# Kernel optimization log

Hardware: AMD Instinct MI355X
Metric: run time of the kernel (lower is better)

## Reference

```python
import jax, jax.numpy as jnp
import numpy as np

N_USERS = 100_000
N_ITEMS = 50_000
E = 2_000_000
B = 100_000
DU, DI, H, L = 256, 128, 64, 2
EPS = 1e-5  # BatchNorm eps


def setup_inputs() -> dict:
    key = jax.random.key(0)
    ks = jax.random.split(key, 32)
    f32 = jnp.float32
    inp = {
        "user_features": jax.random.normal(ks[0], (N_USERS, DU), f32),
        "item_features": jax.random.normal(ks[1], (N_ITEMS, DI), f32),
        "edge_index": jnp.stack([
            jax.random.randint(ks[2], (E,), 0, N_USERS),
            jax.random.randint(ks[3], (E,), 0, N_ITEMS),
        ]).astype(jnp.int32),
        "edge_label_index": jnp.stack([
            jax.random.randint(ks[4], (B,), 0, N_USERS),
            jax.random.randint(ks[5], (B,), 0, N_ITEMS),
        ]).astype(jnp.int32),
        # projections (stored as [in, out])
        "user_proj_W": jax.random.normal(ks[6], (DU, H), f32) * 0.05,
        "user_proj_b": jax.random.normal(ks[7], (H,), f32) * 0.05,
        "item_proj_W": jax.random.normal(ks[8], (DI, H), f32) * 0.05,
        "item_proj_b": jax.random.normal(ks[9], (H,), f32) * 0.05,
        # SAGEConv weights stacked over layers: lin_l (aggr neighbors, with bias), lin_r (self, no bias)
        "u_lin_l_W": jax.random.normal(ks[10], (L, H, H), f32) * 0.1,
        "u_lin_l_b": jax.random.normal(ks[11], (L, H), f32) * 0.05,
        "u_lin_r_W": jax.random.normal(ks[12], (L, H, H), f32) * 0.1,
        "i_lin_l_W": jax.random.normal(ks[13], (L, H, H), f32) * 0.1,
        "i_lin_l_b": jax.random.normal(ks[14], (L, H), f32) * 0.05,
        "i_lin_r_W": jax.random.normal(ks[15], (L, H, H), f32) * 0.1,
        # BatchNorm (eval mode: affine + running stats)
        "u_bn_gamma": 1.0 + jax.random.normal(ks[16], (L, H), f32) * 0.05,
        "u_bn_beta": jax.random.normal(ks[17], (L, H), f32) * 0.05,
        "u_bn_mean": jax.random.normal(ks[18], (L, H), f32) * 0.05,
        "u_bn_var": jax.random.uniform(ks[19], (L, H), f32, 0.5, 1.5),
        "i_bn_gamma": 1.0 + jax.random.normal(ks[20], (L, H), f32) * 0.05,
        "i_bn_beta": jax.random.normal(ks[21], (L, H), f32) * 0.05,
        "i_bn_mean": jax.random.normal(ks[22], (L, H), f32) * 0.05,
        "i_bn_var": jax.random.uniform(ks[23], (L, H), f32, 0.5, 1.5),
        # final MLP head
        "fc1_W": jax.random.normal(ks[24], (2 * H, H), f32) * 0.1,
        "fc1_b": jax.random.normal(ks[25], (H,), f32) * 0.05,
        "fc2_W": jax.random.normal(ks[26], (H, 4), f32) * 0.1,
        "fc2_b": jax.random.normal(ks[27], (4,), f32) * 0.05,
    }
    return inp


def _bn(x, g, b, m, v):
    return (x - m) * (g * jax.lax.rsqrt(v + EPS)) + b


def _forward(user_features, item_features, edge_index, edge_label_index,
             user_proj_W, user_proj_b, item_proj_W, item_proj_b,
             u_lin_l_W, u_lin_l_b, u_lin_r_W,
             i_lin_l_W, i_lin_l_b, i_lin_r_W,
             u_bn_gamma, u_bn_beta, u_bn_mean, u_bn_var,
             i_bn_gamma, i_bn_beta, i_bn_mean, i_bn_var,
             fc1_W, fc1_b, fc2_W, fc2_b):
    src, dst = edge_index[0], edge_index[1]  # user idx, item idx
    ux = user_features @ user_proj_W + user_proj_b  # [Nu, H]
    ix = item_features @ item_proj_W + item_proj_b  # [Ni, H]
    # in-degree of items (for mean aggregation), clamp for isolated nodes
    deg_i = jnp.clip(jax.ops.segment_sum(jnp.ones((E,), ux.dtype), dst, N_ITEMS), 1.0)[:, None]
    for l in range(L):
        # user conv: aggr='max' over item neighbors (edge_index flipped)
        agg_u = jax.ops.segment_max(ix[dst], src, num_segments=N_USERS)
        agg_u = jnp.where(jnp.isfinite(agg_u), agg_u, 0.0)  # empty segments -> 0 (PyG behavior)
        u_new = agg_u @ u_lin_l_W[l] + u_lin_l_b[l] + ux @ u_lin_r_W[l]
        u_new = jax.nn.relu(_bn(u_new, u_bn_gamma[l], u_bn_beta[l], u_bn_mean[l], u_bn_var[l]))
        # item conv: aggr='mean' over user neighbors
        agg_i = jax.ops.segment_sum(ux[src], dst, num_segments=N_ITEMS) / deg_i
        i_new = agg_i @ i_lin_l_W[l] + i_lin_l_b[l] + ix @ i_lin_r_W[l]
        i_new = jax.nn.relu(_bn(i_new, i_bn_gamma[l], i_bn_beta[l], i_bn_mean[l], i_bn_var[l]))
        ux, ix = u_new, i_new
    uh = ux[edge_label_index[0]]  # [B, H]
    ih = ix[edge_label_index[1]]  # [B, H]
    x = jnp.concatenate([uh, ih], axis=1)  # [B, 2H]
    return jax.nn.relu(x @ fc1_W + fc1_b) @ fc2_W + fc2_b  # [B, 4]


def reference(user_features, item_features, edge_index, edge_label_index,
              user_proj_W, user_proj_b, item_proj_W, item_proj_b,
              u_lin_l_W, u_lin_l_b, u_lin_r_W,
              i_lin_l_W, i_lin_l_b, i_lin_r_W,
              u_bn_gamma, u_bn_beta, u_bn_mean, u_bn_var,
              i_bn_gamma, i_bn_beta, i_bn_mean, i_bn_var,
              fc1_W, fc1_b, fc2_W, fc2_b):
    return _forward(user_features, item_features, edge_index, edge_label_index,
                    user_proj_W, user_proj_b, item_proj_W, item_proj_b,
                    u_lin_l_W, u_lin_l_b, u_lin_r_W,
                    i_lin_l_W, i_lin_l_b, i_lin_r_W,
                    u_bn_gamma, u_bn_beta, u_bn_mean, u_bn_var,
                    i_bn_gamma, i_bn_beta, i_bn_mean, i_bn_var,
                    fc1_W, fc1_b, fc2_W, fc2_b)
```

## Files before the change

### kernel.cpp

```cpp
#include <hip/hip_runtime.h>
#include <math.h>

#define N_USERS 100000
#define N_ITEMS 50000
#define NE      2000000
#define NB      100000
#define H       64
#define BN_EPS  1e-5f
#define P_PART  8
#define U_LOC   (N_USERS / P_PART)
#define I_LOC   (N_ITEMS / P_PART)
#define HSLOTS  (U_LOC + I_LOC)
#define S_SLICES 50
#define NBLK_CSR (P_PART * S_SLICES)
#define E_SLICE  (NE / S_SLICES)
#define Q_SLICE  (E_SLICE / 4)
#define SCAN_CHUNK 2048
#define T_CSR   512
#define GU_BLK  ((N_USERS + 127) / 128)
#define GI_BLK  ((N_ITEMS + 127) / 128)

typedef __attribute__((ext_vector_type(8))) short bf16x8;
typedef __attribute__((ext_vector_type(4))) float f32x4;
typedef __attribute__((ext_vector_type(4))) int   i32x4;

static __device__ __forceinline__ int rfl(int x) { return __builtin_amdgcn_readfirstlane(x); }

static __device__ __forceinline__ unsigned short f2bf(float f) {
  union { float f; unsigned u; } v; v.f = f;
  const unsigned r = v.u + 0x7fffu + ((v.u >> 16) & 1u);
  return (unsigned short)(r >> 16);
}
static __device__ __forceinline__ float bf2f(unsigned short h) {
  union { unsigned u; float f; } v; v.u = (unsigned)h << 16;
  return v.f;
}
static __device__ __forceinline__ float bfu_lo(unsigned x) {
  union { unsigned u; float f; } v; v.u = x << 16;
  return v.f;
}
static __device__ __forceinline__ float bfu_hi(unsigned x) {
  union { unsigned u; float f; } v; v.u = x & 0xffff0000u;
  return v.f;
}

__global__ __launch_bounds__(256) void pack_kernel(
    const float* __restrict__ upW, const float* __restrict__ ipW,
    const float* __restrict__ ulW, const float* __restrict__ urW,
    const float* __restrict__ ilW, const float* __restrict__ irW,
    const float* __restrict__ f1W, unsigned short* __restrict__ dst) {
  const int b = blockIdx.x;
  const int ct = threadIdx.x >> 6, lane = threadIdx.x & 63;
  const float* src;
  int krow0;
  if (b < 8)       { src = upW; krow0 = b * 32; }
  else if (b < 12) { src = ipW; krow0 = (b - 8) * 32; }
  else if (b < 28) {
    const int idx = b - 12, t = idx >> 2, ks = idx & 3;
    const int layer = t & 1;
    const float* Wl = (t < 2) ? ulW : ilW;
    const float* Wr = (t < 2) ? urW : irW;
    src = ((ks < 2) ? Wl : Wr) + layer * 4096;
    krow0 = ((ks < 2) ? ks : ks - 2) * 32;
  } else { src = f1W; krow0 = (b - 28) * 32; }
  unsigned short* out = dst + (size_t)b * 2048 + ((size_t)ct * 64 + lane) * 8;
  const int col = ct * 16 + (lane & 15);
  const int kr = krow0 + (lane >> 4) * 8;
#pragma unroll
  for (int j = 0; j < 8; j++) out[j] = f2bf(src[(kr + j) * 64 + col]);
}

template<int K>
static __device__ __forceinline__ void proj_body(
    const float* __restrict__ X, const unsigned short* __restrict__ Wf,
    const float* __restrict__ bias, unsigned short* __restrict__ Y,
    int nrows, int bp) {
  const int lane = threadIdx.x & 63;
  const int wave = rfl((int)(threadIdx.x >> 6));
  const int r0 = (bp * 8 + wave) * 16;
  if (r0 >= nrows) return;
  const int arow = r0 + (lane & 15);
  const int ar = arow < nrows ? arow : nrows - 1;
  const int k0 = (lane >> 4) * 8;
  f32x4 acc[4] = {};
#pragma unroll
  for (int ks = 0; ks < K / 32; ks++) {
    const float* xp = X + (size_t)ar * K + ks * 32 + k0;
    const float4 xa = *reinterpret_cast<const float4*>(xp);
    const float4 xb = *reinterpret_cast<const float4*>(xp + 4);
    bf16x8 af;
    af[0] = f2bf(xa.x); af[1] = f2bf(xa.y); af[2] = f2bf(xa.z); af[3] = f2bf(xa.w);
    af[4] = f2bf(xb.x); af[5] = f2bf(xb.y); af[6] = f2bf(xb.z); af[7] = f2bf(xb.w);
#pragma unroll
    for (int ct = 0; ct < 4; ct++) {
      const bf16x8 bfr = *reinterpret_cast<const bf16x8*>(
          Wf + ((size_t)(ks * 4 + ct) * 64 + lane) * 8);
      acc[ct] = __builtin_amdgcn_mfma_f32_16x16x32_bf16(af, bfr, acc[ct], 0, 0, 0);
    }
  }
  const int orow0 = r0 + (lane >> 4) * 4;
#pragma unroll
  for (int ct = 0; ct < 4; ct++) {
    const int col = ct * 16 + (lane & 15);
    const float bv = bias[col];
#pragma unroll
    for (int i = 0; i < 4; i++) {
      const int r = orow0 + i;
      if (r < nrows) Y[(size_t)r * 64 + col] = f2bf(acc[ct][i] + bv);
    }
  }
}

__global__ __launch_bounds__(T_CSR) void fused_hist_proj(
    const int* __restrict__ src, const int* __restrict__ dst,
    unsigned short* __restrict__ PH,
    const float* __restrict__ userF, const float* __restrict__ itemF,
    const unsigned short* __restrict__ wpack,
    const float* __restrict__ upb, const float* __restrict__ ipb,
    unsigned short* __restrict__ ux0, unsigned short* __restrict__ ix0) {
  __shared__ int h[HSLOTS];
  const int b = blockIdx.x;
  if (b < NBLK_CSR) {
    const int p = b & (P_PART - 1);
    const int s = b >> 3;
    for (int i = threadIdx.x; i < HSLOTS; i += T_CSR) h[i] = 0;
    __syncthreads();
    const int uLo = p * U_LOC, iLo = p * I_LOC;
    const int e0 = s * E_SLICE;
    const i32x4* s4 = reinterpret_cast<const i32x4*>(src + e0);
    const i32x4* d4 = reinterpret_cast<const i32x4*>(dst + e0);
    for (int i = threadIdx.x; i < Q_SLICE; i += T_CSR) {
      const i32x4 us = s4[i];
      const i32x4 ds = d4[i];
#pragma unroll
      for (int q = 0; q < 4; q++) {
        const int ul = us[q] - uLo;
        if ((unsigned)ul < (unsigned)U_LOC) atomicAdd(&h[ul], 1);
        const int il = ds[q] - iLo;
        if ((unsigned)il < (unsigned)I_LOC) atomicAdd(&h[U_LOC + il], 1);
      }
    }
    __syncthreads();
    unsigned short* out = PH + (size_t)b * HSLOTS;
    for (int i = threadIdx.x; i < HSLOTS; i += T_CSR)
      __builtin_nontemporal_store((unsigned short)h[i], &out[i]);
  } else if (b < NBLK_CSR + GU_BLK) {
    proj_body<256>(userF, wpack, upb, ux0, N_USERS, b - NBLK_CSR);
  } else {
    proj_body<128>(itemF, wpack + 8 * 2048, ipb, ix0, N_ITEMS,
                   b - NBLK_CSR - GU_BLK);
  }
}

__global__ __launch_bounds__(256) void conv_mfma(
    const unsigned short* __restrict__ AGG, const unsigned short* __restrict__ XS,
    const unsigned short* __restrict__ Wf, const float* __restrict__ bl,
    const float* __restrict__ gm, const float* __restrict__ bt,
    const float* __restrict__ mu, const float* __restrict__ vr,
    unsigned short* __restrict__ Y, int nrows) {
  const int lane = threadIdx.x & 63;
  const int wave = rfl((int)(threadIdx.x >> 6));
  const int r0 = (blockIdx.x * 4 + wave) * 16;
  if (r0 >= nrows) return;
  const int arow = r0 + (lane & 15);
  const int ar = arow < nrows ? arow : nrows - 1;
  const int k0 = (lane >> 4) * 8;
  f32x4 acc[4] = {};
#pragma unroll
  for (int ks = 0; ks < 4; ks++) {
    const unsigned short* ap =
        (ks < 2 ? AGG : XS) + (size_t)ar * 64 + (ks & 1) * 32 + k0;
    const bf16x8 af = *reinterpret_cast<const bf16x8*>(ap);
#pragma unroll
    for (int ct = 0; ct < 4; ct++) {
      const bf16x8 bfr = *reinterpret_cast<const bf16x8*>(
          Wf + ((size_t)(ks * 4 + ct) * 64 + lane) * 8);
      acc[ct] = __builtin_amdgcn_mfma_f32_16x16x32_bf16(af, bfr, acc[ct], 0, 0, 0);
    }
  }
  const int orow0 = r0 + (lane >> 4) * 4;
#pragma unroll
  for (int ct = 0; ct < 4; ct++) {
    const int col = ct * 16 + (lane & 15);
    const float s = gm[col] * rsqrtf(vr[col] + BN_EPS);
    const float C = (bl[col] - mu[col]) * s + bt[col];
#pragma unroll
    for (int i = 0; i < 4; i++) {
      const int r = orow0 + i;
      if (r < nrows)
        Y[(size_t)r * 64 + col] = f2bf(fmaxf(fmaf(acc[ct][i], s, C), 0.f));
    }
  }
}

__global__ __launch_bounds__(256) void combine_kernel(
    unsigned short* __restrict__ PH, int* __restrict__ cntU,
    int* __restrict__ cntI) {
  const int g = blockIdx.x * 256 + threadIdx.x;
  if (g >= P_PART * HSLOTS) return;
  const int x = g / HSLOTS;
  const int n = g - x * HSLOTS;
  unsigned short* p = PH + (size_t)x * HSLOTS + n;
  int run = 0;
#pragma unroll 2
  for (int s = 0; s < S_SLICES; s++) {
    unsigned short* q = p + (size_t)s * (P_PART * HSLOTS);
    const int v = (int)__builtin_nontemporal_load(q);
    __builtin_nontemporal_store((unsigned short)run, q);
    run += v;
  }
  if (n < U_LOC) cntU[x * U_LOC + n] = run;
  else           cntI[x * I_LOC + (n - U_LOC)] = run;
}

__global__ __launch_bounds__(256) void scan1_kernel(
    const int* __restrict__ cnt, int* __restrict__ row,
    int* __restrict__ bsum, int n) {
  __shared__ int wtot[4];
  const int tid = threadIdx.x;
  const int lane = tid & 63, wv = tid >> 6;
  const int i0 = blockIdx.x * SCAN_CHUNK + tid * 8;
  int sacc[8];
  int run = 0;
#pragma unroll
  for (int k = 0; k < 8; k++) {
    const int v = (i0 + k < n) ? cnt[i0 + k] : 0;
    run += v;
    sacc[k] = run;
  }
  int x = run;
#pragma unroll
  for (int off = 1; off < 64; off <<= 1) {
    const int y = __shfl_up(x, off);
    if (lane >= off) x += y;
  }
  if (lane == 63) wtot[wv] = x;
  __syncthreads();
  int woff = 0;
#pragma unroll
  for (int k = 0; k < 4; k++) woff += (k < wv) ? wtot[k] : 0;
  const int excl = (x - run) + woff;
#pragma unroll
  for (int k = 0; k < 8; k++)
    if (i0 + k < n) row[i0 + k + 1] = excl + sacc[k];
  if (tid == 255) bsum[blockIdx.x] = excl + run;
}

__global__ __launch_bounds__(256) void scan3_kernel(
    const int* __restrict__ bsum, int* __restrict__ row, int n) {
  __shared__ int off_s;
  const int b = blockIdx.x;
  const int tid = threadIdx.x;
  if (tid < 64) {
    int v = (tid < b) ? bsum[tid] : 0;
#pragma unroll
    for (int off = 32; off; off >>= 1) v += __shfl_xor(v, off);
    if (tid == 0) off_s = v;
  }
  __syncthreads();
  const int off = off_s;
  if (b == 0) {
    if (tid == 0) row[0] = 0;
    return;
  }
  const int i0 = b * SCAN_CHUNK + tid * 8;
#pragma unroll
  for (int k = 0; k < 8; k++)
    if (i0 + k < n) row[i0 + k + 1] += off;
}

__global__ __launch_bounds__(T_CSR) void scatter2_kernel(
    const int* __restrict__ src, const int* __restrict__ dst,
    const unsigned short* __restrict__ PH, const int* __restrict__ rowU,
    const int* __restrict__ rowI, int* __restrict__ adjU,
    int* __restrict__ adjI) {
  __shared__ int pos[HSLOTS];
  const int p = blockIdx.x & (P_PART - 1);
  const int s = blockIdx.x >> 3;
  const int uLo = p * U_LOC, iLo = p * I_LOC;
  const unsigned short* pre = PH + (size_t)blockIdx.x * HSLOTS;
  for (int i = threadIdx.x; i < U_LOC; i += T_CSR)
    pos[i] = rowU[uLo + i] + (int)__builtin_nontemporal_load(&pre[i]);
  for (int i = threadIdx.x; i < I_LOC; i += T_CSR)
    pos[U_LOC + i] = rowI[iLo + i] + (int)__builtin_nontemporal_load(&pre[U_LOC + i]);
  __syncthreads();
  const int e0 = s * E_SLICE;
  const i32x4* s4 = reinterpret_cast<const i32x4*>(src + e0);
  const i32x4* d4 = reinterpret_cast<const i32x4*>(dst + e0);
  for (int i = threadIdx.x; i < Q_SLICE; i += T_CSR) {
    const i32x4 us = s4[i];
    const i32x4 ds = d4[i];
#pragma unroll
    for (int q = 0; q < 4; q++) {
      const int u = us[q], it = ds[q];
      const int ul = u - uLo, il = it - iLo;
      if ((unsigned)ul < (unsigned)U_LOC) {
        const int pp = atomicAdd(&pos[ul], 1);
        adjU[pp] = it;
      }
      if ((unsigned)il < (unsigned)I_LOC) {
        const int pp = atomicAdd(&pos[U_LOC + il], 1);
        adjI[pp] = u;
      }
    }
  }
}

__global__ __launch_bounds__(256) void agg_max_kernel(
    const unsigned short* __restrict__ feat, const int* __restrict__ rowptr,
    const int* __restrict__ adj, unsigned short* __restrict__ out, int nseg) {
  const int lane = threadIdx.x & 63;
  const int wid  = rfl((int)(threadIdx.x >> 6));
  const int g    = lane >> 4;
  const int c4   = (lane & 15) * 4;
  for (int s = blockIdx.x * 4 + wid; s < nseg; s += gridDim.x * 4) {
    const int beg = rowptr[s], end = rowptr[s + 1];
    float m0 = -INFINITY, m1 = -INFINITY, m2 = -INFINITY, m3 = -INFINITY;
    float n0 = -INFINITY, n1 = -INFINITY, n2 = -INFINITY, n3 = -INFINITY;
    int j = beg;
    for (; j + 8 <= end; j += 8) {
      const int ia = adj[j + g];
      const int ib = adj[j + 4 + g];
      const uint2 va = *reinterpret_cast<const uint2*>(feat + (size_t)ia * H + c4);
      const uint2 vb = *reinterpret_cast<const uint2*>(feat + (size_t)ib * H + c4);
      m0 = fmaxf(m0, bfu_lo(va.x)); m1 = fmaxf(m1, bfu_hi(va.x));
      m2 = fmaxf(m2, bfu_lo(va.y)); m3 = fmaxf(m3, bfu_hi(va.y));
      n0 = fmaxf(n0, bfu_lo(vb.x)); n1 = fmaxf(n1, bfu_hi(vb.x));
      n2 = fmaxf(n2, bfu_lo(vb.y)); n3 = fmaxf(n3, bfu_hi(vb.y));
    }
    for (; j < end; j += 4) {
      if (j + g < end) {
        const int ia = adj[j + g];
        const uint2 va = *reinterpret_cast<const uint2*>(feat + (size_t)ia * H + c4);
        m0 = fmaxf(m0, bfu_lo(va.x)); m1 = fmaxf(m1, bfu_hi(va.x));
        m2 = fmaxf(m2, bfu_lo(va.y)); m3 = fmaxf(m3, bfu_hi(va.y));
      }
    }
    m0 = fmaxf(m0, n0); m1 = fmaxf(m1, n1);
    m2 = fmaxf(m2, n2); m3 = fmaxf(m3, n3);
    m0 = fmaxf(m0, __shfl_xor(m0, 16)); m0 = fmaxf(m0, __shfl_xor(m0, 32));
    m1 = fmaxf(m1, __shfl_xor(m1, 16)); m1 = fmaxf(m1, __shfl_xor(m1, 32));
    m2 = fmaxf(m2, __shfl_xor(m2, 16)); m2 = fmaxf(m2, __shfl_xor(m2, 32));
    m3 = fmaxf(m3, __shfl_xor(m3, 16)); m3 = fmaxf(m3, __shfl_xor(m3, 32));
    if (lane < 16) {
      uint2 o;
      if (end > beg) {
        o.x = (unsigned)f2bf(m0) | ((unsigned)f2bf(m1) << 16);
        o.y = (unsigned)f2bf(m2) | ((unsigned)f2bf(m3) << 16);
      } else {
        o.x = 0; o.y = 0;
      }
      *reinterpret_cast<uint2*>(out + (size_t)s * H + c4) = o;
    }
  }
}

__global__ __launch_bounds__(256) void agg_mean_kernel(
    const unsigned short* __restrict__ feat, const int* __restrict__ rowptr,
    const int* __restrict__ adj, unsigned short* __restrict__ out, int nseg) {
  const int lane = threadIdx.x & 63;
  const int wid  = rfl((int)(threadIdx.x >> 6));
  const int g    = lane >> 4;
  const int c4   = (lane & 15) * 4;
  for (int s = blockIdx.x * 4 + wid; s < nseg; s += gridDim.x * 4) {
    const int beg = rowptr[s], end = rowptr[s + 1];
    float a0 = 0.f, a1 = 0.f, a2 = 0.f, a3 = 0.f;
    float b0 = 0.f, b1 = 0.f, b2 = 0.f, b3 = 0.f;
    int j = beg;
    for (; j + 8 <= end; j += 8) {
      const int ia = adj[j + g];
      const int ib = adj[j + 4 + g];
      const uint2 va = *reinterpret_cast<const uint2*>(feat + (size_t)ia * H + c4);
      const uint2 vb = *reinterpret_cast<const uint2*>(feat + (size_t)ib * H + c4);
      a0 += bfu_lo(va.x); a1 += bfu_hi(va.x);
      a2 += bfu_lo(va.y); a3 += bfu_hi(va.y);
      b0 += bfu_lo(vb.x); b1 += bfu_hi(vb.x);
      b2 += bfu_lo(vb.y); b3 += bfu_hi(vb.y);
    }
    for (; j < end; j += 4) {
      if (j + g < end) {
        const int ia = adj[j + g];
        const uint2 va = *reinterpret_cast<const uint2*>(feat + (size_t)ia * H + c4);
        a0 += bfu_lo(va.x); a1 += bfu_hi(va.x);
        a2 += bfu_lo(va.y); a3 += bfu_hi(va.y);
      }
    }
    a0 += b0; a1 += b1; a2 += b2; a3 += b3;
    a0 += __shfl_xor(a0, 16); a0 += __shfl_xor(a0, 32);
    a1 += __shfl_xor(a1, 16); a1 += __shfl_xor(a1, 32);
    a2 += __shfl_xor(a2, 16); a2 += __shfl_xor(a2, 32);
    a3 += __shfl_xor(a3, 16); a3 += __shfl_xor(a3, 32);
    if (lane < 16) {
      const float inv = 1.f / (float)((end - beg) > 1 ? (end - beg) : 1);
      uint2 o;
      o.x = (unsigned)f2bf(a0 * inv) | ((unsigned)f2bf(a1 * inv) << 16);
      o.y = (unsigned)f2bf(a2 * inv) | ((unsigned)f2bf(a3 * inv) << 16);
      *reinterpret_cast<uint2*>(out + (size_t)s * H + c4) = o;
    }
  }
}

__global__ __launch_bounds__(256) void head_mfma(
    const unsigned short* __restrict__ ux, const unsigned short* __restrict__ ix,
    const int* __restrict__ eliU, const int* __restrict__ eliI,
    const unsigned short* __restrict__ W1f, const float* __restrict__ b1,
    const float* __restrict__ W2, const float* __restrict__ b2,
    float* __restrict__ out) {
  const int lane = threadIdx.x & 63;
  const int wave = rfl((int)(threadIdx.x >> 6));
  const int r0 = (blockIdx.x * 4 + wave) * 16;
  if (r0 >= NB) return;
  const int rr = r0 + (lane & 15);
  const int rc = rr < NB ? rr : NB - 1;
  const int idxU = eliU[rc], idxI = eliI[rc];
  const int k0 = (lane >> 4) * 8;
  f32x4 acc[4] = {};
#pragma unroll
  for (int ks = 0; ks < 4; ks++) {
    const unsigned short* ap = (ks < 2)
        ? ux + (size_t)idxU * 64 + (ks & 1) * 32 + k0
        : ix + (size_t)idxI * 64 + (ks & 1) * 32 + k0;
    const bf16x8 af = *reinterpret_cast<const bf16x8*>(ap);
#pragma unroll
    for (int ct = 0; ct < 4; ct++) {
      const bf16x8 bfr = *reinterpret_cast<const bf16x8*>(
          W1f + ((size_t)(ks * 4 + ct) * 64 + lane) * 8);
      acc[ct] = __builtin_amdgcn_mfma_f32_16x16x32_bf16(af, bfr, acc[ct], 0, 0, 0);
    }
  }
  float p[4][4];
#pragma unroll
  for (int i = 0; i < 4; i++)
#pragma unroll
    for (int o = 0; o < 4; o++) p[i][o] = 0.f;
#pragma unroll
  for (int ct = 0; ct < 4; ct++) {
    const int col = ct * 16 + (lane & 15);
    const float bb = b1[col];
    const float wa = W2[col * 4 + 0], wb = W2[col * 4 + 1];
    const float wc = W2[col * 4 + 2], wd = W2[col * 4 + 3];
#pragma unroll
    for (int i = 0; i < 4; i++) {
      const float h = fmaxf(acc[ct][i] + bb, 0.f);
      p[i][0] = fmaf(h, wa, p[i][0]);
      p[i][1] = fmaf(h, wb, p[i][1]);
      p[i][2] = fmaf(h, wc, p[i][2]);
      p[i][3] = fmaf(h, wd, p[i][3]);
    }
  }
#pragma unroll
  for (int off = 1; off < 16; off <<= 1) {
#pragma unroll
    for (int i = 0; i < 4; i++) {
      p[i][0] += __shfl_xor(p[i][0], off);
      p[i][1] += __shfl_xor(p[i][1], off);
      p[i][2] += __shfl_xor(p[i][2], off);
      p[i][3] += __shfl_xor(p[i][3], off);
    }
  }
  if ((lane & 15) == 0) {
    const int row0 = r0 + (lane >> 4) * 4;
#pragma unroll
    for (int i = 0; i < 4; i++) {
      const int r = row0 + i;
      if (r < NB) {
        float4 o4 = { p[i][0] + b2[0], p[i][1] + b2[1],
                      p[i][2] + b2[2], p[i][3] + b2[3] };
        *reinterpret_cast<float4*>(out + (size_t)r * 4) = o4;
      }
    }
  }
}

extern "C" void kernel_launch(void* const* d_in, const int* in_sizes, int n_in,
                              void* d_out, int out_size, void* d_ws, size_t ws_size,
                              hipStream_t stream) {
  const float* userF = (const float*)d_in[0];
  const float* itemF = (const float*)d_in[1];
  const int*   src   = (const int*)d_in[2];
  const int*   dst   = src + NE;
  const int*   eliU  = (const int*)d_in[3];
  const int*   eliI  = eliU + NB;
  const float* upW = (const float*)d_in[4],  *upb = (const float*)d_in[5];
  const float* ipW = (const float*)d_in[6],  *ipb = (const float*)d_in[7];
  const float* ulW = (const float*)d_in[8],  *ulb = (const float*)d_in[9];
  const float* urW = (const float*)d_in[10];
  const float* ilW = (const float*)d_in[11], *ilb = (const float*)d_in[12];
  const float* irW = (const float*)d_in[13];
  const float* ug  = (const float*)d_in[14], *ube = (const float*)d_in[15];
  const float* um  = (const float*)d_in[16], *uv  = (const float*)d_in[17];
  const float* ig  = (const float*)d_in[18], *ibe = (const float*)d_in[19];
  const float* im  = (const float*)d_in[20], *iv  = (const float*)d_in[21];
  const float* f1W = (const float*)d_in[22], *f1b = (const float*)d_in[23];
  const float* f2W = (const float*)d_in[24], *f2b = (const float*)d_in[25];
  float* outp = (float*)d_out;

  char* p = (char*)d_ws;
  auto alloc = [&](size_t bytes) {
    char* r = p;
    p += (bytes + 255) & ~(size_t)255;
    return r;
  };
  unsigned short* ux0 = (unsigned short*)alloc((size_t)N_USERS * H * 2);
  unsigned short* ix0 = (unsigned short*)alloc((size_t)N_ITEMS * H * 2);
  char* grp = alloc((size_t)38400 * 1024);
  unsigned short* agU = (unsigned short*)grp;
  unsigned short* agI = agU + (size_t)N_USERS * H;
  unsigned short* ux1 = agI + (size_t)N_ITEMS * H;
  unsigned short* ix1 = ux1 + (size_t)N_USERS * H;
  unsigned short* PH = (unsigned short*)grp;
  int*   rowU = (int*)alloc((size_t)(N_USERS + 1) * 4);
  int*   rowI = (int*)alloc((size_t)(N_ITEMS + 1) * 4);
  int*   cntU = (int*)alloc((size_t)N_USERS * 4);
  int*   cntI = (int*)alloc((size_t)N_ITEMS * 4);
  int*   adjU = (int*)alloc((size_t)NE * 4);
  int*   adjI = (int*)alloc((size_t)NE * 4);
  int*   bsumU = (int*)alloc(64 * 4);
  int*   bsumI = (int*)alloc(64 * 4);
  unsigned short* wpack = (unsigned short*)alloc((size_t)32 * 2048 * 2);

  const int G = 2048, T = 256;
  const int SBU = (N_USERS + SCAN_CHUNK - 1) / SCAN_CHUNK;
  const int SBI = (N_ITEMS + SCAN_CHUNK - 1) / SCAN_CHUNK;
  pack_kernel<<<32, T, 0, stream>>>(upW, ipW, ulW, urW, ilW, irW, f1W, wpack);
  fused_hist_proj<<<NBLK_CSR + GU_BLK + GI_BLK, T_CSR, 0, stream>>>(
      src, dst, PH, userF, itemF, wpack, upb, ipb, ux0, ix0);
  combine_kernel<<<(P_PART * HSLOTS + 255) / 256, T, 0, stream>>>(PH, cntU, cntI);
  scan1_kernel<<<SBU, T, 0, stream>>>(cntU, rowU, bsumU, N_USERS);
  scan1_kernel<<<SBI, T, 0, stream>>>(cntI, rowI, bsumI, N_ITEMS);
  scan3_kernel<<<SBU, T, 0, stream>>>(bsumU, rowU, N_USERS);
  scan3_kernel<<<SBI, T, 0, stream>>>(bsumI, rowI, N_ITEMS);
  scatter2_kernel<<<NBLK_CSR, T_CSR, 0, stream>>>(src, dst, PH, rowU, rowI, adjU, adjI);

  const unsigned short* uin = ux0;
  const unsigned short* iin = ix0;
  unsigned short* uout = ux1;
  unsigned short* iout = ix1;
  const int GU = (N_USERS + 63) / 64, GI = (N_ITEMS + 63) / 64;
  for (int l = 0; l < 2; l++) {
    unsigned short* cwU = wpack + (12 + 4 * (0 + l)) * 2048;
    unsigned short* cwI = wpack + (12 + 4 * (2 + l)) * 2048;
    agg_max_kernel<<<G, T, 0, stream>>>(iin, rowU, adjU, agU, N_USERS);
    conv_mfma<<<GU, T, 0, stream>>>(agU, uin, cwU, ulb + l * 64,
                                    ug + l * 64, ube + l * 64,
                                    um + l * 64, uv + l * 64, uout, N_USERS);
    agg_mean_kernel<<<G, T, 0, stream>>>(uin, rowI, adjI, agI, N_ITEMS);
    conv_mfma<<<GI, T, 0, stream>>>(agI, iin, cwI, ilb + l * 64,
                                    ig + l * 64, ibe + l * 64,
                                    im + l * 64, iv + l * 64, iout, N_ITEMS);
    const unsigned short* t;
    t = uin; uin = uout; uout = (unsigned short*)t;
    t = iin; iin = iout; iout = (unsigned short*)t;
  }
  head_mfma<<<(NB / 16 + 3) / 4, T, 0, stream>>>(uin, iin, eliU, eliI,
                                                 wpack + 28 * 2048, f1b, f2W, f2b, outp);
}
```

Baseline: 368.3 us.

## Split neighbor aggregation into two column-half passes with nontemporal index loads

```diff
diff --git a/kernel.cpp b/kernel.cpp
--- a/kernel.cpp
+++ b/kernel.cpp
@@ -308,19 +308,20 @@
 
 __global__ __launch_bounds__(256) void agg_max_kernel(
     const unsigned short* __restrict__ feat, const int* __restrict__ rowptr,
-    const int* __restrict__ adj, unsigned short* __restrict__ out, int nseg) {
+    const int* __restrict__ adj, unsigned short* __restrict__ out,
+    int nseg, int coff) {
   const int lane = threadIdx.x & 63;
   const int wid  = rfl((int)(threadIdx.x >> 6));
-  const int g    = lane >> 4;
-  const int c4   = (lane & 15) * 4;
+  const int g    = lane >> 3;
+  const int c4   = ((lane & 7) << 2) + coff;
   for (int s = blockIdx.x * 4 + wid; s < nseg; s += gridDim.x * 4) {
     const int beg = rowptr[s], end = rowptr[s + 1];
     float m0 = -INFINITY, m1 = -INFINITY, m2 = -INFINITY, m3 = -INFINITY;
     float n0 = -INFINITY, n1 = -INFINITY, n2 = -INFINITY, n3 = -INFINITY;
     int j = beg;
-    for (; j + 8 <= end; j += 8) {
-      const int ia = adj[j + g];
-      const int ib = adj[j + 4 + g];
+    for (; j + 16 <= end; j += 16) {
+      const int ia = __builtin_nontemporal_load(&adj[j + g]);
+      const int ib = __builtin_nontemporal_load(&adj[j + 8 + g]);
       const uint2 va = *reinterpret_cast<const uint2*>(feat + (size_t)ia * H + c4);
       const uint2 vb = *reinterpret_cast<const uint2*>(feat + (size_t)ib * H + c4);
       m0 = fmaxf(m0, bfu_lo(va.x)); m1 = fmaxf(m1, bfu_hi(va.x));
@@ -328,9 +329,9 @@
       n0 = fmaxf(n0, bfu_lo(vb.x)); n1 = fmaxf(n1, bfu_hi(vb.x));
       n2 = fmaxf(n2, bfu_lo(vb.y)); n3 = fmaxf(n3, bfu_hi(vb.y));
     }
-    for (; j < end; j += 4) {
+    for (; j < end; j += 8) {
       if (j + g < end) {
-        const int ia = adj[j + g];
+        const int ia = __builtin_nontemporal_load(&adj[j + g]);
         const uint2 va = *reinterpret_cast<const uint2*>(feat + (size_t)ia * H + c4);
         m0 = fmaxf(m0, bfu_lo(va.x)); m1 = fmaxf(m1, bfu_hi(va.x));
         m2 = fmaxf(m2, bfu_lo(va.y)); m3 = fmaxf(m3, bfu_hi(va.y));
@@ -338,38 +339,42 @@
     }
     m0 = fmaxf(m0, n0); m1 = fmaxf(m1, n1);
     m2 = fmaxf(m2, n2); m3 = fmaxf(m3, n3);
-    m0 = fmaxf(m0, __shfl_xor(m0, 16)); m0 = fmaxf(m0, __shfl_xor(m0, 32));
-    m1 = fmaxf(m1, __shfl_xor(m1, 16)); m1 = fmaxf(m1, __shfl_xor(m1, 32));
-    m2 = fmaxf(m2, __shfl_xor(m2, 16)); m2 = fmaxf(m2, __shfl_xor(m2, 32));
-    m3 = fmaxf(m3, __shfl_xor(m3, 16)); m3 = fmaxf(m3, __shfl_xor(m3, 32));
-    if (lane < 16) {
-      uint2 o;
+#pragma unroll
+    for (int off = 8; off <= 32; off <<= 1) {
+      m0 = fmaxf(m0, __shfl_xor(m0, off));
+      m1 = fmaxf(m1, __shfl_xor(m1, off));
+      m2 = fmaxf(m2, __shfl_xor(m2, off));
+      m3 = fmaxf(m3, __shfl_xor(m3, off));
+    }
+    if (lane < 8) {
+      unsigned long long o = 0ull;
       if (end > beg) {
-        o.x = (unsigned)f2bf(m0) | ((unsigned)f2bf(m1) << 16);
-        o.y = (unsigned)f2bf(m2) | ((unsigned)f2bf(m3) << 16);
-      } else {
-        o.x = 0; o.y = 0;
-      }
-      *reinterpret_cast<uint2*>(out + (size_t)s * H + c4) = o;
+        const unsigned lo = (unsigned)f2bf(m0) | ((unsigned)f2bf(m1) << 16);
+        const unsigned hi = (unsigned)f2bf(m2) | ((unsigned)f2bf(m3) << 16);
+        o = (unsigned long long)lo | ((unsigned long long)hi << 32);
+      }
+      __builtin_nontemporal_store(
+          o, reinterpret_cast<unsigned long long*>(out + (size_t)s * H + c4));
     }
   }
 }
 
 __global__ __launch_bounds__(256) void agg_mean_kernel(
     const unsigned short* __restrict__ feat, const int* __restrict__ rowptr,
-    const int* __restrict__ adj, unsigned short* __restrict__ out, int nseg) {
+    const int* __restrict__ adj, unsigned short* __restrict__ out,
+    int nseg, int coff) {
   const int lane = threadIdx.x & 63;
   const int wid  = rfl((int)(threadIdx.x >> 6));
-  const int g    = lane >> 4;
-  const int c4   = (lane & 15) * 4;
+  const int g    = lane >> 3;
+  const int c4   = ((lane & 7) << 2) + coff;
   for (int s = blockIdx.x * 4 + wid; s < nseg; s += gridDim.x * 4) {
     const int beg = rowptr[s], end = rowptr[s + 1];
     float a0 = 0.f, a1 = 0.f, a2 = 0.f, a3 = 0.f;
     float b0 = 0.f, b1 = 0.f, b2 = 0.f, b3 = 0.f;
     int j = beg;
-    for (; j + 8 <= end; j += 8) {
-      const int ia = adj[j + g];
-      const int ib = adj[j + 4 + g];
+    for (; j + 16 <= end; j += 16) {
+      const int ia = __builtin_nontemporal_load(&adj[j + g]);
+      const int ib = __builtin_nontemporal_load(&adj[j + 8 + g]);
       const uint2 va = *reinterpret_cast<const uint2*>(feat + (size_t)ia * H + c4);
       const uint2 vb = *reinterpret_cast<const uint2*>(feat + (size_t)ib * H + c4);
       a0 += bfu_lo(va.x); a1 += bfu_hi(va.x);
@@ -377,25 +382,30 @@
       b0 += bfu_lo(vb.x); b1 += bfu_hi(vb.x);
       b2 += bfu_lo(vb.y); b3 += bfu_hi(vb.y);
     }
-    for (; j < end; j += 4) {
+    for (; j < end; j += 8) {
       if (j + g < end) {
-        const int ia = adj[j + g];
+        const int ia = __builtin_nontemporal_load(&adj[j + g]);
         const uint2 va = *reinterpret_cast<const uint2*>(feat + (size_t)ia * H + c4);
         a0 += bfu_lo(va.x); a1 += bfu_hi(va.x);
         a2 += bfu_lo(va.y); a3 += bfu_hi(va.y);
       }
     }
     a0 += b0; a1 += b1; a2 += b2; a3 += b3;
-    a0 += __shfl_xor(a0, 16); a0 += __shfl_xor(a0, 32);
-    a1 += __shfl_xor(a1, 16); a1 += __shfl_xor(a1, 32);
-    a2 += __shfl_xor(a2, 16); a2 += __shfl_xor(a2, 32);
-    a3 += __shfl_xor(a3, 16); a3 += __shfl_xor(a3, 32);
-    if (lane < 16) {
+#pragma unroll
+    for (int off = 8; off <= 32; off <<= 1) {
+      a0 += __shfl_xor(a0, off);
+      a1 += __shfl_xor(a1, off);
+      a2 += __shfl_xor(a2, off);
+      a3 += __shfl_xor(a3, off);
+    }
+    if (lane < 8) {
       const float inv = 1.f / (float)((end - beg) > 1 ? (end - beg) : 1);
-      uint2 o;
-      o.x = (unsigned)f2bf(a0 * inv) | ((unsigned)f2bf(a1 * inv) << 16);
-      o.y = (unsigned)f2bf(a2 * inv) | ((unsigned)f2bf(a3 * inv) << 16);
-      *reinterpret_cast<uint2*>(out + (size_t)s * H + c4) = o;
+      const unsigned lo = (unsigned)f2bf(a0 * inv) | ((unsigned)f2bf(a1 * inv) << 16);
+      const unsigned hi = (unsigned)f2bf(a2 * inv) | ((unsigned)f2bf(a3 * inv) << 16);
+      const unsigned long long o =
+          (unsigned long long)lo | ((unsigned long long)hi << 32);
+      __builtin_nontemporal_store(
+          o, reinterpret_cast<unsigned long long*>(out + (size_t)s * H + c4));
     }
   }
 }
@@ -540,11 +550,13 @@
   for (int l = 0; l < 2; l++) {
     unsigned short* cwU = wpack + (12 + 4 * (0 + l)) * 2048;
     unsigned short* cwI = wpack + (12 + 4 * (2 + l)) * 2048;
-    agg_max_kernel<<<G, T, 0, stream>>>(iin, rowU, adjU, agU, N_USERS);
+    agg_max_kernel<<<G, T, 0, stream>>>(iin, rowU, adjU, agU, N_USERS, 0);
+    agg_max_kernel<<<G, T, 0, stream>>>(iin, rowU, adjU, agU, N_USERS, 32);
     conv_mfma<<<GU, T, 0, stream>>>(agU, uin, cwU, ulb + l * 64,
                                     ug + l * 64, ube + l * 64,
                                     um + l * 64, uv + l * 64, uout, N_USERS);
-    agg_mean_kernel<<<G, T, 0, stream>>>(uin, rowI, adjI, agI, N_ITEMS);
+    agg_mean_kernel<<<G, T, 0, stream>>>(uin, rowI, adjI, agI, N_ITEMS, 0);
+    agg_mean_kernel<<<G, T, 0, stream>>>(uin, rowI, adjI, agI, N_ITEMS, 32);
     conv_mfma<<<GI, T, 0, stream>>>(agI, iin, cwI, ilb + l * 64,
                                     ig + l * 64, ibe + l * 64,
                                     im + l * 64, iv + l * 64, iout, N_ITEMS);
```

After: 491.7 us. +33.5%, slower.
